# Optimization experiments

Hardware: AMD Instinct MI355X
Metric: run time of the kernel (lower is better)

The kernel has to match this reference:

```python
import jax, jax.numpy as jnp
import numpy as np

B, N, C = 8, 2_000_000, 16


def _per_batch_loss(x, t, num_classes):
    """x: [N] float values, t: [N] int labels.
    For each label group: loss = mean(group) - mode(group) (scipy mode,
    ties -> smallest value), scattered back to every position of that label.
    """
    n = x.shape[0]
    # Sort primarily by label, secondarily by value (lexsort: last key primary).
    order = jnp.lexsort((x, t))
    xs = x[order]
    ts = t[order]
    # Run-length encode equal (label, value) pairs to count value multiplicity.
    new_run = jnp.concatenate(
        [jnp.ones((1,), bool), (ts[1:] != ts[:-1]) | (xs[1:] != xs[:-1])])
    run_id = jnp.cumsum(new_run) - 1                      # [N]
    run_cnt = jax.ops.segment_sum(jnp.ones(n, xs.dtype), run_id,
                                  num_segments=n)[run_id]  # count per element
    # Mode per label = smallest value attaining the max multiplicity.
    grp_max = jax.ops.segment_max(run_cnt, ts, num_segments=num_classes)
    mode = jax.ops.segment_min(
        jnp.where(run_cnt == grp_max[ts], xs, jnp.inf), ts,
        num_segments=num_classes)                         # [C]
    ssum = jax.ops.segment_sum(xs, ts, num_segments=num_classes)
    scnt = jax.ops.segment_sum(jnp.ones(n, xs.dtype), ts,
                               num_segments=num_classes)
    mean = ssum / jnp.maximum(scnt, 1.0)
    per_label = jnp.where(scnt > 0, mean - mode, 0.0)     # [C]
    return per_label[t]                                    # scatter back, [N]


def setup_inputs() -> dict:
    key = jax.random.key(0)
    k1, k2 = jax.random.split(key)
    inputs = jax.random.normal(k1, (B, N), dtype=jnp.float32)
    targets = jax.random.randint(k2, (B, N), 0, C, dtype=jnp.int32)
    return {"inputs": inputs, "targets": targets, "num_classes": C}


def reference(inputs, targets, num_classes):
    per_pos = jax.vmap(lambda x, t: _per_batch_loss(x, t, num_classes))(
        inputs, targets)                                   # [B, N]
    return jnp.mean(per_pos)
```

## Files before the change

### kernel.cpp

```cpp
#include <hip/hip_runtime.h>
#include <stdint.h>

#define NUM_C 16
#define NUM_B 8
#define NPAIR 512
#define CHUNK_S 8192
#define HALF_S (CHUNK_S / 2)
#define TAB 8192
#define MAX_NB 8

__device__ __forceinline__ unsigned hash_u32(unsigned h) {
    h ^= h >> 16; h *= 0x85ebca6bu;
    h ^= h >> 13; h *= 0xc2b2ae35u;
    h ^= h >> 16;
    return h;
}
__device__ __forceinline__ unsigned canon_key(float v) {
    unsigned k = __float_as_uint(v);
    return (k == 0x80000000u) ? 0u : k;
}
__device__ __forceinline__ unsigned pair_of(unsigned key, int c) {
    return ((unsigned)c << 5) | (hash_u32(key) >> 27);
}

__global__ void __launch_bounds__(512)
hist_kernel(const float* __restrict__ x, const int* __restrict__ t,
            long long N, int bbase, int nchunk,
            unsigned short* __restrict__ counts, unsigned char* __restrict__ t8)
{
    __shared__ unsigned hist[NPAIR];
    const int lb = blockIdx.x / nchunk;
    const int ch = blockIdx.x % nchunk;
    const int b  = bbase + lb;
    const long long base = (long long)ch * CHUNK_S;
    const int count = (int)((N - base < CHUNK_S) ? (N - base) : CHUNK_S);
    const float* xb = x + (size_t)b * N + base;
    const int*   tb = t + (size_t)b * N + base;
    unsigned char* t8b = t8 + (size_t)lb * N + base;
    const int tid = threadIdx.x;

    hist[tid] = 0u;
    __syncthreads();

    const bool vec_ok = ((N & 3) == 0);
    const int n4 = vec_ok ? (count >> 2) : 0;
    #pragma unroll
    for (int r = 0; r < 4; ++r) {
        const int i = tid + r * 512;
        if (i < n4) {
            float4 v  = ((const float4*)xb)[i];
            int4   cc = ((const int4*)tb)[i];
            atomicAdd(&hist[pair_of(canon_key(v.x), cc.x)], 1u);
            atomicAdd(&hist[pair_of(canon_key(v.y), cc.y)], 1u);
            atomicAdd(&hist[pair_of(canon_key(v.z), cc.z)], 1u);
            atomicAdd(&hist[pair_of(canon_key(v.w), cc.w)], 1u);
            uchar4 q;
            q.x = (unsigned char)cc.x; q.y = (unsigned char)cc.y;
            q.z = (unsigned char)cc.z; q.w = (unsigned char)cc.w;
            ((uchar4*)t8b)[i] = q;
        }
    }
    for (int i = (n4 << 2) + tid; i < count; i += 512) {
        int c = tb[i];
        atomicAdd(&hist[pair_of(canon_key(xb[i]), c)], 1u);
        t8b[i] = (unsigned char)c;
    }
    __syncthreads();
    counts[((size_t)lb * nchunk + ch) * NPAIR + tid] = (unsigned short)hist[tid];
}

__global__ void __launch_bounds__(512)
scan_kernel(const unsigned short* __restrict__ counts,
            unsigned* __restrict__ gpos, unsigned* __restrict__ ptot,
            int nchunk)
{
    __shared__ unsigned short tile[256][32];
    __shared__ unsigned part[16][32];
    const int lb = blockIdx.x >> 4;
    const int c0 = (blockIdx.x & 15) * 32;
    const int tid = threadIdx.x;
    const unsigned short* cb = counts + (size_t)lb * nchunk * NPAIR;

    for (int i = tid; i < 256 * 32; i += 512) {
        int r = i >> 5, cc = i & 31;
        tile[r][cc] = (r < nchunk)
            ? cb[(size_t)r * NPAIR + c0 + cc] : (unsigned short)0;
    }
    __syncthreads();

    const int col = tid & 31, seg = tid >> 5;
    unsigned ssum = 0;
    #pragma unroll
    for (int r = 0; r < 16; ++r) ssum += tile[seg * 16 + r][col];
    part[seg][col] = ssum;
    __syncthreads();
    if (seg == 0) {
        unsigned run = 0;
        #pragma unroll
        for (int j = 0; j < 16; ++j) {
            unsigned v = part[j][col]; part[j][col] = run; run += v;
        }
        ptot[(size_t)lb * NPAIR + c0 + col] = run;
    }
    __syncthreads();
    unsigned run = part[seg][col];
    unsigned* gp = gpos + (size_t)lb * nchunk * NPAIR;
    #pragma unroll
    for (int r = 0; r < 16; ++r) {
        int rr = seg * 16 + r;
        if (rr < nchunk) gp[(size_t)rr * NPAIR + c0 + col] = run;
        run += tile[rr][col];
    }
}

__global__ void __launch_bounds__(512)
base_kernel(const unsigned* __restrict__ ptot, unsigned* __restrict__ pbase)
{
    __shared__ unsigned wsum[8];
    const int lb = blockIdx.x, tid = threadIdx.x, lane = tid & 63;
    unsigned v = ptot[(size_t)lb * NPAIR + tid];
    unsigned inc = v;
    #pragma unroll
    for (int d = 1; d < 64; d <<= 1) {
        unsigned tt = __shfl_up(inc, d);
        if (lane >= d) inc += tt;
    }
    if (lane == 63) wsum[tid >> 6] = inc;
    __syncthreads();
    unsigned wbase = 0;
    for (int i = 0; i < (tid >> 6); ++i) wbase += wsum[i];
    unsigned excl = wbase + inc - v;
    unsigned* pb = pbase + (size_t)lb * (NPAIR + 1);
    pb[tid] = excl;
    if (tid == NPAIR - 1) pb[NPAIR] = excl + v;
}

__global__ void __launch_bounds__(512)
place_kernel(const float* __restrict__ x, const unsigned char* __restrict__ t8,
             long long N, int bbase, int nchunk,
             const unsigned* __restrict__ gpos, const unsigned* __restrict__ pbase,
             unsigned* __restrict__ keysout)
{
    __shared__ unsigned lout[HALF_S];
    __shared__ unsigned short rid[HALF_S];
    __shared__ unsigned hist[NPAIR];
    __shared__ unsigned delta[NPAIR];
    __shared__ unsigned wsum[8];

    const int lb = blockIdx.x / nchunk;
    const int ch = blockIdx.x % nchunk;
    const int b  = bbase + lb;
    const long long base = (long long)ch * CHUNK_S;
    const int count = (int)((N - base < CHUNK_S) ? (N - base) : CHUNK_S);
    const float* xb = x + (size_t)b * N + base;
    const unsigned char* t8b = t8 + (size_t)lb * N + base;
    const int tid = threadIdx.x;
    const int lane = tid & 63;

    const unsigned pg = pbase[(size_t)lb * (NPAIR + 1) + tid]
                      + gpos[((size_t)lb * nchunk + ch) * NPAIR + tid];
    unsigned carry = 0u;
    unsigned* kb = keysout + (size_t)lb * N;
    const bool vec_ok = ((N & 3) == 0);

    for (int h = 0; h < 2; ++h) {
        const int i0 = h * HALF_S;
        const int hc = ((count - i0) < HALF_S) ? (count - i0) : HALF_S;
        if (hc <= 0) break;
        hist[tid] = 0u;
        __syncthreads();

        unsigned keyr[8], rp[8];
        #pragma unroll
        for (int j = 0; j < 8; ++j) rp[j] = 0xFFFFFFFFu;
        if (vec_ok) {
            const int n4 = hc >> 2;
            #pragma unroll
            for (int r2 = 0; r2 < 2; ++r2) {
                const int idx4 = tid + r2 * 512;
                if (idx4 < n4) {
                    float4 v  = ((const float4*)(xb + i0))[idx4];
                    uchar4 cc = ((const uchar4*)(t8b + i0))[idx4];
                    unsigned k0 = canon_key(v.x), g0 = pair_of(k0, cc.x);
                    unsigned k1 = canon_key(v.y), g1 = pair_of(k1, cc.y);
                    unsigned k2 = canon_key(v.z), g2 = pair_of(k2, cc.z);
                    unsigned k3 = canon_key(v.w), g3 = pair_of(k3, cc.w);
                    unsigned p0 = atomicAdd(&hist[g0], 1u);
                    unsigned p1 = atomicAdd(&hist[g1], 1u);
                    unsigned p2 = atomicAdd(&hist[g2], 1u);
                    unsigned p3 = atomicAdd(&hist[g3], 1u);
                    keyr[r2*4+0] = k0; rp[r2*4+0] = (g0 << 16) | p0;
                    keyr[r2*4+1] = k1; rp[r2*4+1] = (g1 << 16) | p1;
                    keyr[r2*4+2] = k2; rp[r2*4+2] = (g2 << 16) | p2;
                    keyr[r2*4+3] = k3; rp[r2*4+3] = (g3 << 16) | p3;
                }
            }
        } else {
            #pragma unroll
            for (int j = 0; j < 8; ++j) {
                const int i = tid + j * 512;
                if (i < hc) {
                    unsigned k = canon_key(xb[i0 + i]);
                    unsigned g = pair_of(k, (int)t8b[i0 + i]);
                    unsigned p = atomicAdd(&hist[g], 1u);
                    keyr[j] = k; rp[j] = (g << 16) | p;
                }
            }
        }
        __syncthreads();

        unsigned v = hist[tid], inc = v;
        #pragma unroll
        for (int d = 1; d < 64; d <<= 1) {
            unsigned tt = __shfl_up(inc, d);
            if (lane >= d) inc += tt;
        }
        if (lane == 63) wsum[tid >> 6] = inc;
        __syncthreads();
        unsigned wbase = 0;
        for (int i = 0; i < (tid >> 6); ++i) wbase += wsum[i];
        const unsigned excl = wbase + inc - v;
        hist[tid]  = excl;
        delta[tid] = pg + carry - excl;
        carry += v;
        __syncthreads();

        #pragma unroll
        for (int j = 0; j < 8; ++j) {
            if (rp[j] != 0xFFFFFFFFu) {
                const unsigned g = rp[j] >> 16, p = rp[j] & 0xFFFFu;
                const unsigned idx = hist[g] + p;
                lout[idx] = keyr[j];
                rid[idx]  = (unsigned short)g;
            }
        }
        __syncthreads();

        for (int i = tid; i < hc; i += 512) {
            const unsigned g = rid[i];
            kb[delta[g] + (unsigned)i] = lout[i];
        }
        __syncthreads();
    }
}

__global__ void __launch_bounds__(512)
mode_kernel(const unsigned* __restrict__ keysout,
            const unsigned* __restrict__ pbase, long long N, int bbase,
            unsigned long long* __restrict__ best,
            double* __restrict__ psum,
            unsigned* __restrict__ pcnt)
{
    __shared__ unsigned keyt[TAB];
    __shared__ unsigned cnt16[TAB / 2];
    __shared__ unsigned long long redb[8];
    __shared__ double reds[8];

    const unsigned lb = blockIdx.x >> 9;
    const unsigned pr = blockIdx.x & 511u;
    const unsigned c  = pr >> 5;
    const unsigned b  = (unsigned)bbase + lb;
    const int tid = threadIdx.x;
    const int lane = tid & 63, wid = tid >> 6;

    const uint4 z4 = make_uint4(0u, 0u, 0u, 0u);
    for (int i = tid; i < TAB / 4; i += 512) ((uint4*)keyt)[i] = z4;
    for (int i = tid; i < TAB / 8; i += 512) ((uint4*)cnt16)[i] = z4;
    __syncthreads();

    const unsigned* pb = pbase + (size_t)lb * (NPAIR + 1);
    const unsigned s = pb[pr], e = pb[pr + 1];
    const unsigned* kb = keysout + (size_t)lb * N;

    double ls = 0.0;
    unsigned mo = 0xFFFFFFFFu;
    unsigned bc = 0u, bo = 0xFFFFFFFFu;

    for (unsigned j4 = s + (unsigned)tid * 4u; j4 < e; j4 += 2048u) {
        const int nv = (int)((e - j4 < 4u) ? (e - j4) : 4u);
        unsigned kk[4];
        #pragma unroll
        for (int m = 0; m < 4; ++m)
            kk[m] = (m < nv) ? kb[j4 + (unsigned)m] : 0u;
        unsigned od[4], h[4], old[4];
        int dh[4];
        #pragma unroll
        for (int m = 0; m < 4; ++m) {
            dh[m] = 0;
            if (m < nv) {
                unsigned key = kk[m];
                ls += (double)__uint_as_float(key);
                unsigned o = (key & 0x80000000u) ? ~key : (key | 0x80000000u);
                if (o < mo) mo = o;
                od[m] = o;
                h[m] = hash_u32(o) & (TAB - 1);
                dh[m] = (j4 + (unsigned)m - s) < (unsigned)TAB;
            }
        }
        #pragma unroll
        for (int m = 0; m < 4; ++m)
            if (dh[m]) old[m] = atomicCAS(&keyt[h[m]], 0u, od[m]);
        #pragma unroll
        for (int m = 0; m < 4; ++m) {
            if (!dh[m]) continue;
            unsigned o = old[m], hh = h[m];
            const unsigned oo = od[m];
            unsigned cnt = 1u;
            while (o != 0u) {
                if (o == oo) {
                    unsigned sh = (hh & 1u) << 4;
                    unsigned ret = atomicAdd(&cnt16[hh >> 1], 1u << sh);
                    cnt = ((ret >> sh) & 0xFFFFu) + 2u;
                    break;
                }
                hh = (hh + 1u) & (TAB - 1u);
                o = atomicCAS(&keyt[hh], 0u, oo);
            }
            if (cnt >= 2u && (cnt > bc || (cnt == bc && oo < bo))) {
                bc = cnt; bo = oo;
            }
        }
    }

    unsigned long long lbst = bc ? (((unsigned long long)bc << 32)
                                    | (unsigned long long)(~bo)) : 0ull;
    {
        unsigned long long s1 = (1ull << 32) | (unsigned long long)(~mo);
        if (s1 > lbst) lbst = s1;
    }
    #pragma unroll
    for (int sh = 32; sh > 0; sh >>= 1) {
        unsigned long long obv = __shfl_down(lbst, sh);
        if (obv > lbst) lbst = obv;
        ls += __shfl_down(ls, sh);
    }
    if (lane == 0) { redb[wid] = lbst; reds[wid] = ls; }
    __syncthreads();
    if (tid == 0) {
        unsigned long long bb = 0ull; double ss = 0.0;
        #pragma unroll
        for (int i = 0; i < 8; ++i) {
            if (redb[i] > bb) bb = redb[i];
            ss += reds[i];
        }
        psum[b * NPAIR + pr] = ss;
        pcnt[b * NPAIR + pr] = e - s;
        if (bb) atomicMax(&best[b * NUM_C + c], bb);
    }
}

__global__ void __launch_bounds__(128)
finalize_kernel(const double* __restrict__ psum,
                const unsigned* __restrict__ pcnt,
                const unsigned long long* __restrict__ best,
                float* __restrict__ out, double inv_total)
{
    __shared__ double acc[NUM_B * NUM_C];
    const int i = threadIdx.x;
    const int b = i >> 4, c = i & 15;

    double s = 0.0;
    unsigned long long cnt = 0ull;
    const double*   ps = psum + (size_t)b * NPAIR + ((size_t)c << 5);
    const unsigned* pc = pcnt + (size_t)b * NPAIR + ((size_t)c << 5);
    for (int r = 0; r < 32; ++r) { s += ps[r]; cnt += pc[r]; }

    double term = 0.0;
    if (cnt > 0ull) {
        unsigned long long p = best[i];
        unsigned ord = 0xFFFFFFFFu - (unsigned)(p & 0xFFFFFFFFull);
        unsigned ub  = (ord & 0x80000000u) ? (ord ^ 0x80000000u) : ~ord;
        float mode = __uint_as_float(ub);
        term = s - (double)cnt * (double)mode;
    }
    acc[i] = term;
    __syncthreads();
    for (int st = 64; st > 0; st >>= 1) {
        if (i < st) acc[i] += acc[i + st];
        __syncthreads();
    }
    if (i == 0) out[0] = (float)(acc[0] * inv_total);
}

extern "C" void kernel_launch(void* const* d_in, const int* in_sizes, int n_in,
                              void* d_out, int out_size, void* d_ws, size_t ws_size,
                              hipStream_t stream)
{
    const float* x = (const float*)d_in[0];
    const int*   t = (const int*)d_in[1];

    const long long total = in_sizes[0];
    const long long N = total / NUM_B;
    const int nchunk = (int)((N + CHUNK_S - 1) / CHUNK_S);

    char* ws = (char*)d_ws;
    size_t off = 0;
    unsigned long long* best = (unsigned long long*)(ws + off);
    off += (size_t)NUM_B * NUM_C * 8;
    double* psum = (double*)(ws + off);
    off += (size_t)NUM_B * NPAIR * 8;
    unsigned* pcnt = (unsigned*)(ws + off);
    off += (size_t)NUM_B * NPAIR * 4;
    off = (off + 255) & ~(size_t)255;

    const size_t keys_per_b  = (size_t)N * 4;
    const size_t t8_per_b    = (size_t)N;
    const size_t cnts_per_b  = (size_t)nchunk * NPAIR * 2;
    const size_t gpos_per_b  = (size_t)nchunk * NPAIR * 4;
    const size_t ptot_per_b  = (size_t)NPAIR * 4;
    const size_t pbase_per_b = (size_t)(NPAIR + 1) * 4;
    const size_t per_b = keys_per_b + t8_per_b + cnts_per_b + gpos_per_b
                       + ptot_per_b + pbase_per_b + 1024;
    size_t remaining = ws_size - off;
    int nb = (int)(remaining / per_b);
    if (nb < 1) nb = 1;
    if (nb > MAX_NB) nb = MAX_NB;
    {
        int rounds = (NUM_B + nb - 1) / nb;
        nb = (NUM_B + rounds - 1) / rounds;
    }

    unsigned* keysout = (unsigned*)(ws + off);
    off += (size_t)nb * keys_per_b;
    off = (off + 255) & ~(size_t)255;
    unsigned short* counts = (unsigned short*)(ws + off);
    off += (size_t)nb * cnts_per_b;
    off = (off + 255) & ~(size_t)255;
    unsigned* gpos = (unsigned*)(ws + off);
    off += (size_t)nb * gpos_per_b;
    off = (off + 255) & ~(size_t)255;
    unsigned* ptot = (unsigned*)(ws + off);
    off += (size_t)nb * ptot_per_b;
    off = (off + 255) & ~(size_t)255;
    unsigned* pbase = (unsigned*)(ws + off);
    off += (size_t)nb * pbase_per_b;
    off = (off + 255) & ~(size_t)255;
    unsigned char* t8 = (unsigned char*)(ws + off);
    off += (size_t)nb * t8_per_b;

    hipMemsetAsync(best, 0, (size_t)NUM_B * NUM_C * 8, stream);
    for (int r = 0; r < NUM_B; r += nb) {
        const int nbr = (NUM_B - r < nb) ? (NUM_B - r) : nb;
        hist_kernel<<<nbr * nchunk, 512, 0, stream>>>(
            x, t, N, r, nchunk, counts, t8);
        scan_kernel<<<nbr * 16, 512, 0, stream>>>(
            counts, gpos, ptot, nchunk);
        base_kernel<<<nbr, 512, 0, stream>>>(ptot, pbase);
        place_kernel<<<nbr * nchunk, 512, 0, stream>>>(
            x, t8, N, r, nchunk, gpos, pbase, keysout);
        mode_kernel<<<nbr * NPAIR, 512, 0, stream>>>(
            keysout, pbase, N, r, best, psum, pcnt);
    }
    finalize_kernel<<<1, 128, 0, stream>>>(
        psum, pcnt, best, (float*)d_out,
        1.0 / ((double)NUM_B * (double)N));
}
```

Before: 286.8 us.

## Double hash partitions per label to shrink per-partition mode tables

Partitions per batch go from 512 to 1024: each label now gets 64 hash buckets instead of 32, and the mode kernel's shared hash table halves from 8192 to 4096 entries. Histogram, scan, base and place kernels now handle two buckets per thread, and the grid sizes are adjusted to match. The aim is to launch more, smaller mode blocks that use less LDS, which should allow more blocks per CU and cut table-clearing cost. The cost is larger counts and gpos arrays, more scan work, and more LDS atomic and scatter bookkeeping in the place kernel.

```diff
diff --git a/kernel.cpp b/kernel.cpp
--- a/kernel.cpp
+++ b/kernel.cpp
@@ -3,10 +3,10 @@
 
 #define NUM_C 16
 #define NUM_B 8
-#define NPAIR 512
+#define NPAIR 1024
 #define CHUNK_S 8192
 #define HALF_S (CHUNK_S / 2)
-#define TAB 8192
+#define TAB 4096
 #define MAX_NB 8
 
 __device__ __forceinline__ unsigned hash_u32(unsigned h) {
@@ -20,7 +20,7 @@
     return (k == 0x80000000u) ? 0u : k;
 }
 __device__ __forceinline__ unsigned pair_of(unsigned key, int c) {
-    return ((unsigned)c << 5) | (hash_u32(key) >> 27);
+    return ((unsigned)c << 6) | (hash_u32(key) >> 26);
 }
 
 __global__ void __launch_bounds__(512)
@@ -39,7 +39,7 @@
     unsigned char* t8b = t8 + (size_t)lb * N + base;
     const int tid = threadIdx.x;
 
-    hist[tid] = 0u;
+    hist[tid] = 0u; hist[tid + 512] = 0u;
     __syncthreads();
 
     const bool vec_ok = ((N & 3) == 0);
@@ -66,7 +66,9 @@
         t8b[i] = (unsigned char)c;
     }
     __syncthreads();
-    counts[((size_t)lb * nchunk + ch) * NPAIR + tid] = (unsigned short)hist[tid];
+    unsigned short* cr = counts + ((size_t)lb * nchunk + ch) * NPAIR;
+    cr[tid]       = (unsigned short)hist[tid];
+    cr[tid + 512] = (unsigned short)hist[tid + 512];
 }
 
 __global__ void __launch_bounds__(512)
@@ -76,8 +78,8 @@
 {
     __shared__ unsigned short tile[256][32];
     __shared__ unsigned part[16][32];
-    const int lb = blockIdx.x >> 4;
-    const int c0 = (blockIdx.x & 15) * 32;
+    const int lb = blockIdx.x >> 5;
+    const int c0 = (blockIdx.x & 31) * 32;
     const int tid = threadIdx.x;
     const unsigned short* cb = counts + (size_t)lb * nchunk * NPAIR;
 
@@ -118,8 +120,9 @@
 {
     __shared__ unsigned wsum[8];
     const int lb = blockIdx.x, tid = threadIdx.x, lane = tid & 63;
-    unsigned v = ptot[(size_t)lb * NPAIR + tid];
-    unsigned inc = v;
+    const unsigned* tr = ptot + (size_t)lb * NPAIR;
+    unsigned b0 = tr[2 * tid], b1 = tr[2 * tid + 1];
+    unsigned s = b0 + b1, inc = s;
     #pragma unroll
     for (int d = 1; d < 64; d <<= 1) {
         unsigned tt = __shfl_up(inc, d);
@@ -129,10 +132,11 @@
     __syncthreads();
     unsigned wbase = 0;
     for (int i = 0; i < (tid >> 6); ++i) wbase += wsum[i];
-    unsigned excl = wbase + inc - v;
+    unsigned excl = wbase + inc - s;
     unsigned* pb = pbase + (size_t)lb * (NPAIR + 1);
-    pb[tid] = excl;
-    if (tid == NPAIR - 1) pb[NPAIR] = excl + v;
+    pb[2 * tid]     = excl;
+    pb[2 * tid + 1] = excl + b0;
+    if (tid == 511) pb[NPAIR] = excl + s;
 }
 
 __global__ void __launch_bounds__(512)
@@ -157,9 +161,11 @@
     const int tid = threadIdx.x;
     const int lane = tid & 63;
 
-    const unsigned pg = pbase[(size_t)lb * (NPAIR + 1) + tid]
-                      + gpos[((size_t)lb * nchunk + ch) * NPAIR + tid];
-    unsigned carry = 0u;
+    const unsigned* pbr = pbase + (size_t)lb * (NPAIR + 1);
+    const unsigned* gpr = gpos + ((size_t)lb * nchunk + ch) * NPAIR;
+    const unsigned pg0 = pbr[2 * tid]     + gpr[2 * tid];
+    const unsigned pg1 = pbr[2 * tid + 1] + gpr[2 * tid + 1];
+    unsigned carry0 = 0u, carry1 = 0u;
     unsigned* kb = keysout + (size_t)lb * N;
     const bool vec_ok = ((N & 3) == 0);
 
@@ -167,7 +173,7 @@
         const int i0 = h * HALF_S;
         const int hc = ((count - i0) < HALF_S) ? (count - i0) : HALF_S;
         if (hc <= 0) break;
-        hist[tid] = 0u;
+        hist[tid] = 0u; hist[tid + 512] = 0u;
         __syncthreads();
 
         unsigned keyr[8], rp[8];
@@ -209,7 +215,8 @@
         }
         __syncthreads();
 
-        unsigned v = hist[tid], inc = v;
+        unsigned v0 = hist[2 * tid], v1 = hist[2 * tid + 1];
+        unsigned s = v0 + v1, inc = s;
         #pragma unroll
         for (int d = 1; d < 64; d <<= 1) {
             unsigned tt = __shfl_up(inc, d);
@@ -219,10 +226,13 @@
         __syncthreads();
         unsigned wbase = 0;
         for (int i = 0; i < (tid >> 6); ++i) wbase += wsum[i];
-        const unsigned excl = wbase + inc - v;
-        hist[tid]  = excl;
-        delta[tid] = pg + carry - excl;
-        carry += v;
+        const unsigned excl0 = wbase + inc - s;
+        const unsigned excl1 = excl0 + v0;
+        hist[2 * tid]      = excl0;
+        hist[2 * tid + 1]  = excl1;
+        delta[2 * tid]     = pg0 + carry0 - excl0;
+        delta[2 * tid + 1] = pg1 + carry1 - excl1;
+        carry0 += v0; carry1 += v1;
         __syncthreads();
 
         #pragma unroll
@@ -256,9 +266,9 @@
     __shared__ unsigned long long redb[8];
     __shared__ double reds[8];
 
-    const unsigned lb = blockIdx.x >> 9;
-    const unsigned pr = blockIdx.x & 511u;
-    const unsigned c  = pr >> 5;
+    const unsigned lb = blockIdx.x >> 10;
+    const unsigned pr = blockIdx.x & 1023u;
+    const unsigned c  = pr >> 6;
     const unsigned b  = (unsigned)bbase + lb;
     const int tid = threadIdx.x;
     const int lane = tid & 63, wid = tid >> 6;
@@ -361,9 +371,9 @@
 
     double s = 0.0;
     unsigned long long cnt = 0ull;
-    const double*   ps = psum + (size_t)b * NPAIR + ((size_t)c << 5);
-    const unsigned* pc = pcnt + (size_t)b * NPAIR + ((size_t)c << 5);
-    for (int r = 0; r < 32; ++r) { s += ps[r]; cnt += pc[r]; }
+    const double*   ps = psum + (size_t)b * NPAIR + ((size_t)c << 6);
+    const unsigned* pc = pcnt + (size_t)b * NPAIR + ((size_t)c << 6);
+    for (int r = 0; r < 64; ++r) { s += ps[r]; cnt += pc[r]; }
 
     double term = 0.0;
     if (cnt > 0ull) {
@@ -443,7 +453,7 @@
         const int nbr = (NUM_B - r < nb) ? (NUM_B - r) : nb;
         hist_kernel<<<nbr * nchunk, 512, 0, stream>>>(
             x, t, N, r, nchunk, counts, t8);
-        scan_kernel<<<nbr * 16, 512, 0, stream>>>(
+        scan_kernel<<<nbr * 32, 512, 0, stream>>>(
             counts, gpos, ptot, nchunk);
         base_kernel<<<nbr, 512, 0, stream>>>(ptot, pbase);
         place_kernel<<<nbr * nchunk, 512, 0, stream>>>(
```

After: 315.4 us. 9.9% more time.
